# Kernel tuning notes

Hardware: AMD Instinct MI355X
Metric: run time of the kernel (lower is better)

Reference implementation:

```python
import math
import jax, jax.numpy as jnp
import numpy as np

D_MODEL = 256
N_HEADS = 4
HEAD_DIM = D_MODEL // N_HEADS
MAX_REL = 30


def _rel_pos_encodings(t, d_model):
    # sinusoidal table over clipped relative distances -> [t, t, d_model]
    n = 2 * MAX_REL + 1
    positions = jnp.arange(n, dtype=jnp.float32)[:, None]
    div_term = jnp.exp(jnp.arange(0, d_model, 2, dtype=jnp.float32) * (-math.log(10000.0) / d_model))
    ang = positions * div_term                      # [n, d/2]
    enc = jnp.stack([jnp.sin(ang), jnp.cos(ang)], axis=-1).reshape(n, d_model)
    rng = jnp.arange(t)
    final_mat = jnp.clip(rng[None, :] - rng[:, None], -MAX_REL, MAX_REL) + MAX_REL  # [t, t]
    return enc[final_mat]                           # [t, t, d_model]


def setup_inputs() -> dict:
    key = jax.random.key(0)
    ks = jax.random.split(key, 12)
    d = D_MODEL
    s = 1.0 / math.sqrt(d)
    inp = {
        "inputs": jax.random.normal(ks[0], (16, 512, d), dtype=jnp.float32),
        "ln_gamma": jnp.ones((d,), jnp.float32),
        "ln_beta": jnp.zeros((d,), jnp.float32),
        "Wq": jax.random.normal(ks[1], (d, d), jnp.float32) * s,
        "bq": jnp.zeros((d,), jnp.float32),
        "Wk": jax.random.normal(ks[2], (d, d), jnp.float32) * s,
        "bk": jnp.zeros((d,), jnp.float32),
        "Wv": jax.random.normal(ks[3], (d, d), jnp.float32) * s,
        "bv": jnp.zeros((d,), jnp.float32),
        "Wpos": jax.random.normal(ks[4], (d, d), jnp.float32) * s,
        "bpos": jnp.zeros((d,), jnp.float32),
        "Wo": jax.random.normal(ks[5], (d, d), jnp.float32) * s,
        "bo": jnp.zeros((d,), jnp.float32),
        "u_bias": jax.random.normal(ks[6], (1, N_HEADS, 1, HEAD_DIM), jnp.float32) * 0.02,
        "v_bias": jax.random.normal(ks[7], (1, N_HEADS, 1, HEAD_DIM), jnp.float32) * 0.02,
    }
    return inp


def reference(inputs, ln_gamma, ln_beta, Wq, bq, Wk, bk, Wv, bv, Wpos, bpos, Wo, bo, u_bias, v_bias):
    b, t, d = inputs.shape
    h, hd = N_HEADS, HEAD_DIM
    # LayerNorm (eps=1e-5, torch default)
    mu = jnp.mean(inputs, axis=-1, keepdims=True)
    var = jnp.mean(jnp.square(inputs - mu), axis=-1, keepdims=True)
    x = (inputs - mu) * jax.lax.rsqrt(var + 1e-5) * ln_gamma + ln_beta

    def split_heads(y):
        return y.reshape(b, t, h, hd).transpose(0, 2, 1, 3)  # b h t d

    q = split_heads(x @ Wq.T + bq)
    k = split_heads(x @ Wk.T + bk)
    v = split_heads(x @ Wv.T + bv)

    rel = jax.lax.stop_gradient(_rel_pos_encodings(t, d))    # [t, t, d]
    pos = (rel @ Wpos.T + bpos).reshape(t, t, h, hd)         # [t1, t2, h, hd]

    qk_score = jnp.einsum('bhtd,bhsd->bhts', q + u_bias, k)
    pos_score = jnp.einsum('bhtd,tshd->bhts', q + v_bias, pos)
    scores = (qk_score + pos_score) / math.sqrt(hd)
    attn = jax.nn.softmax(scores, axis=-1)
    ctx = jnp.einsum('bhts,bhsd->bhtd', attn, v)
    ctx = ctx.transpose(0, 2, 1, 3).reshape(b, t, d)
    return ctx @ Wo.T + bo
```

## Files before the change

### kernel.cpp

```cpp
#include <hip/hip_runtime.h>
#include <hip/hip_bf16.h>
#include <math.h>

#define B 16
#define T 512
#define D 256
#define H 4
#define HD 64
#define MAXREL 30
#define NREL 61
#define M_ROWS (B*T)
#define QBLK 64

typedef __attribute__((ext_vector_type(8))) short bf16x8;
typedef __attribute__((ext_vector_type(4))) float f32x4;
typedef unsigned short ush;

__device__ inline ush f2b(float f) {
    __hip_bfloat16 h = __float2bfloat16(f);
    union { __hip_bfloat16 h; ush u; } c; c.h = h; return c.u;
}
__device__ inline float b2f(ush u) {
    union { ush u; __hip_bfloat16 h; } c; c.u = u; return __bfloat162float(c.h);
}
__device__ inline int swz(int row, int byteoff) {
    return row * 128 + (byteoff ^ ((row & 7) << 4));
}
__device__ inline int swz256(int row, int byteoff) {
    return row * 256 + (byteoff ^ ((row & 7) << 4));
}
__device__ inline int swz512(int row, int byteoff) {
    return row * 512 + (byteoff ^ ((row & 7) << 4));
}

#define SCL 0.1803368801111204f

__global__ __launch_bounds__(256) void prep_kernel(const float* __restrict__ x,
                                                   const float* __restrict__ gamma,
                                                   const float* __restrict__ beta,
                                                   ush* __restrict__ xb,
                                                   const float* __restrict__ Wq, const float* __restrict__ Wk,
                                                   const float* __restrict__ Wv, const float* __restrict__ Wo,
                                                   ush* __restrict__ wb,
                                                   const float* __restrict__ Wpos,
                                                   const float* __restrict__ bpos,
                                                   ush* __restrict__ pospb) {
    __shared__ __attribute__((aligned(16))) ush wpS[64 * 256];
    int bid = blockIdx.x;
    int tid = threadIdx.x;
    if (bid < 2048) {
        int row = bid * 4 + (tid >> 6);
        int lane = tid & 63;
        const float* xr = x + (size_t)row * D;
        float4 v = *(const float4*)(xr + lane * 4);
        float s = v.x + v.y + v.z + v.w;
        #pragma unroll
        for (int off = 32; off; off >>= 1) s += __shfl_xor(s, off);
        float mu = s * (1.f / 256.f);
        float dx = v.x - mu, dy = v.y - mu, dz = v.z - mu, dw = v.w - mu;
        float vs = dx*dx + dy*dy + dz*dz + dw*dw;
        #pragma unroll
        for (int off = 32; off; off >>= 1) vs += __shfl_xor(vs, off);
        float rstd = rsqrtf(vs * (1.f / 256.f) + 1e-5f);
        float4 g = *(const float4*)(gamma + lane * 4);
        float4 bb = *(const float4*)(beta + lane * 4);
        ushort4 o;
        o.x = f2b(dx * rstd * g.x + bb.x);
        o.y = f2b(dy * rstd * g.y + bb.y);
        o.z = f2b(dz * rstd * g.z + bb.z);
        o.w = f2b(dw * rstd * g.w + bb.w);
        *(ushort4*)(xb + (size_t)row * D + lane * 4) = o;
    } else if (bid < 2048 + 256) {
        int b2 = bid - 2048;
        int z = b2 >> 6, xblk = b2 & 63;
        const float* src = z == 0 ? Wq : z == 1 ? Wk : z == 2 ? Wv : Wo;
        int idx = (xblk * 256 + tid) * 4;
        float4 v = *(const float4*)(src + idx);
        ushort4 o;
        o.x = f2b(v.x); o.y = f2b(v.y); o.z = f2b(v.z); o.w = f2b(v.w);
        *(ushort4*)(wb + (size_t)z * 65536 + idx) = o;
    } else {
        int h = bid - 2304;
        int w = tid >> 6, l = tid & 63, lg = l >> 4, ln = l & 15;
        const float* wsrc = Wpos + (size_t)(h * 64) * D;
        #pragma unroll
        for (int c = 0; c < 16; ++c) {
            int idx = c * 256 + tid;
            int row = idx >> 6, col = (idx & 63) * 4;
            float4 v = *(const float4*)(wsrc + (size_t)row * D + col);
            ushort4 o; o.x = f2b(v.x); o.y = f2b(v.y); o.z = f2b(v.z); o.w = f2b(v.w);
            *(ushort4*)((char*)wpS + swz512(row, col * 2)) = o;
        }
        int p = w * 16 + ln;
        bf16x8 af[8];
        #pragma unroll
        for (int ks = 0; ks < 8; ++ks) {
            #pragma unroll
            for (int j = 0; j < 8; ++j) {
                int k = ks * 32 + lg * 8 + j;
                int i = k >> 1;
                float dt = __expf(-(2.f * i) * (9.210340371976184f / 256.f));
                float ang = (float)p * dt;
                float v = (k & 1) ? __cosf(ang) : __sinf(ang);
                af[ks][j] = (short)f2b(v);
            }
        }
        __syncthreads();
        f32x4 acc[4] = {};
        #pragma unroll
        for (int ks = 0; ks < 8; ++ks) {
            int kbyte = (ks * 32 + lg * 8) * 2;
            #pragma unroll
            for (int ct = 0; ct < 4; ++ct) {
                bf16x8 bf = *(const bf16x8*)((const char*)wpS + swz512(ct * 16 + ln, kbyte));
                acc[ct] = __builtin_amdgcn_mfma_f32_16x16x32_bf16(af[ks], bf, acc[ct], 0, 0, 0);
            }
        }
        #pragma unroll
        for (int ct = 0; ct < 4; ++ct) {
            int dcol = ct * 16 + ln;
            float bb = bpos[h * 64 + dcol];
            #pragma unroll
            for (int r = 0; r < 4; ++r) {
                int pr = w * 16 + lg * 4 + r;
                pospb[(size_t)h * 4096 + pr * 64 + dcol] = f2b(acc[ct][r] + bb);
            }
        }
    }
}

#define PROJ_CORE \
    f32x4 acc[4][4] = {}; \
    { const ush* Ap = A + (size_t)i0 * D; \
      const ush* Wp = W + (size_t)j0 * D; \
      _Pragma("unroll 1") \
      for (int kb2 = 0; kb2 < 2; ++kb2) { \
        int k0 = kb2 * 128; \
        if (kb2) __syncthreads(); \
        _Pragma("unroll") \
        for (int c = 0; c < 8; ++c) { \
            int ci = c * 256 + tid; \
            int row = ci >> 4, sub = ci & 15; \
            *(bf16x8*)((char*)A_s + swz256(row, sub * 16)) = *(const bf16x8*)(Ap + (size_t)row * D + k0 + sub * 8); \
            *(bf16x8*)((char*)B_s + swz256(row, sub * 16)) = *(const bf16x8*)(Wp + (size_t)row * D + k0 + sub * 8); \
        } \
        __syncthreads(); \
        const char* aSrc = swap ? (const char*)A_s : (const char*)B_s; \
        const char* bSrc = swap ? (const char*)B_s : (const char*)A_s; \
        __builtin_amdgcn_s_setprio(1); \
        _Pragma("unroll") \
        for (int ksub = 0; ksub < 4; ++ksub) { \
            int kbyte = ksub * 64 + (l >> 4) * 16; \
            bf16x8 af[4], bfr[4]; \
            _Pragma("unroll") \
            for (int mi = 0; mi < 4; ++mi) af[mi]  = *(const bf16x8*)(aSrc + swz256(wr * 64 + mi * 16 + (l & 15), kbyte)); \
            _Pragma("unroll") \
            for (int ni = 0; ni < 4; ++ni) bfr[ni] = *(const bf16x8*)(bSrc + swz256(wc * 64 + ni * 16 + (l & 15), kbyte)); \
            _Pragma("unroll") \
            for (int mi = 0; mi < 4; ++mi) \
                _Pragma("unroll") \
                for (int ni = 0; ni < 4; ++ni) \
                    acc[mi][ni] = __builtin_amdgcn_mfma_f32_16x16x32_bf16(af[mi], bfr[ni], acc[mi][ni], 0, 0, 0); \
        } \
        __builtin_amdgcn_s_setprio(0); \
      } }

__global__ __launch_bounds__(256, 2) void qkv_mfma(const ush* __restrict__ A,
                                                   const ush* __restrict__ wball,
                                                   const float* __restrict__ bq,
                                                   const float* __restrict__ bk,
                                                   const float* __restrict__ bv,
                                                   ush* __restrict__ qb,
                                                   ush* __restrict__ kbuf,
                                                   ush* __restrict__ vtb) {
    __shared__ __attribute__((aligned(16))) ush A_s[128 * 128];
    __shared__ __attribute__((aligned(16))) ush B_s[128 * 128];
    int tid = threadIdx.x;
    int w = tid >> 6, l = tid & 63;
    int wr = w >> 1, wc = w & 1;
    int i0 = blockIdx.x * 128, j0 = blockIdx.y * 128;
    int z = blockIdx.z;
    const ush* W = wball + (size_t)z * 65536;
    const float* bias = z == 0 ? bq : (z == 1 ? bk : bv);
    int swap = (z == 2) ? 1 : 0;
    PROJ_CORE
    if (swap) {
        #pragma unroll
        for (int mi = 0; mi < 4; ++mi) {
            int t = i0 + wr * 64 + mi * 16 + (l >> 4) * 4;
            #pragma unroll
            for (int ni = 0; ni < 4; ++ni) {
                int j = j0 + wc * 64 + ni * 16 + (l & 15);
                float bvv = bias[j];
                ushort4 o;
                o.x = f2b(acc[mi][ni][0] + bvv); o.y = f2b(acc[mi][ni][1] + bvv);
                o.z = f2b(acc[mi][ni][2] + bvv); o.w = f2b(acc[mi][ni][3] + bvv);
                *(ushort4*)(vtb + (size_t)j * M_ROWS + t) = o;
            }
        }
    } else {
        ush* ob = (z == 0) ? qb : kbuf;
        #pragma unroll
        for (int mi = 0; mi < 4; ++mi) {
            int jb = j0 + wr * 64 + mi * 16 + (l >> 4) * 4;
            float4 bv4 = *(const float4*)(bias + jb);
            #pragma unroll
            for (int ni = 0; ni < 4; ++ni) {
                int t = i0 + wc * 64 + ni * 16 + (l & 15);
                ushort4 o;
                o.x = f2b(acc[mi][ni][0] + bv4.x); o.y = f2b(acc[mi][ni][1] + bv4.y);
                o.z = f2b(acc[mi][ni][2] + bv4.z); o.w = f2b(acc[mi][ni][3] + bv4.w);
                *(ushort4*)(ob + (size_t)t * D + jb) = o;
            }
        }
    }
}

__global__ __launch_bounds__(256, 2) void outproj_mfma(const ush* __restrict__ A,
                                                       const ush* __restrict__ W,
                                                       const float* __restrict__ bias,
                                                       float* __restrict__ of) {
    __shared__ __attribute__((aligned(16))) ush A_s[128 * 128];
    __shared__ __attribute__((aligned(16))) ush B_s[128 * 128];
    int tid = threadIdx.x;
    int w = tid >> 6, l = tid & 63;
    int wr = w >> 1, wc = w & 1;
    int i0 = blockIdx.x * 128, j0 = blockIdx.y * 128;
    const int swap = 0;
    PROJ_CORE
    #pragma unroll
    for (int mi = 0; mi < 4; ++mi) {
        int jb = j0 + wr * 64 + mi * 16 + (l >> 4) * 4;
        float4 bv4 = *(const float4*)(bias + jb);
        #pragma unroll
        for (int ni = 0; ni < 4; ++ni) {
            int t = i0 + wc * 64 + ni * 16 + (l & 15);
            float4 o;
            o.x = acc[mi][ni][0] + bv4.x; o.y = acc[mi][ni][1] + bv4.y;
            o.z = acc[mi][ni][2] + bv4.z; o.w = acc[mi][ni][3] + bv4.w;
            *(float4*)(of + (size_t)t * D + jb) = o;
        }
    }
}

__global__ __launch_bounds__(256, 3) void attn_mfma(const ush* __restrict__ qb,
                                                    const ush* __restrict__ kb,
                                                    const ush* __restrict__ vtb,
                                                    const ush* __restrict__ pospb,
                                                    const float* __restrict__ u_bias,
                                                    const float* __restrict__ v_bias,
                                                    ush* __restrict__ ctxb) {
    __shared__ __attribute__((aligned(16))) ush Kd[2][64 * 64];
    __shared__ __attribute__((aligned(16))) ush Vd[2][64 * 64];
    __shared__ __attribute__((aligned(16))) ush pdS[4][16 * 66];
    __shared__ __attribute__((aligned(16))) ush PlS[4][16 * 64];

    int tid = threadIdx.x;
    int w = tid >> 6;
    int l = tid & 63;
    int lg = l >> 4, ln = l & 15;
    int bh = blockIdx.x;
    int b = bh >> 2, h = bh & 3;
    int t0 = blockIdx.y * QBLK;
    const size_t baseBH = ((size_t)b * T) * D + h * HD;

    bf16x8 qu[2], qv[2];
    {
        const ush* qrow = qb + baseBH + (size_t)(t0 + w * 16 + ln) * D;
        int c0 = lg * 8;
        #pragma unroll
        for (int ks = 0; ks < 2; ++ks) {
            bf16x8 ld = *(const bf16x8*)(qrow + ks * 32 + c0);
            float4 ub0 = *(const float4*)(u_bias + h * HD + ks * 32 + c0);
            float4 ub1 = *(const float4*)(u_bias + h * HD + ks * 32 + c0 + 4);
            float4 vb0 = *(const float4*)(v_bias + h * HD + ks * 32 + c0);
            float4 vb1 = *(const float4*)(v_bias + h * HD + ks * 32 + c0 + 4);
            float ubv[8] = {ub0.x,ub0.y,ub0.z,ub0.w,ub1.x,ub1.y,ub1.z,ub1.w};
            float vbv[8] = {vb0.x,vb0.y,vb0.z,vb0.w,vb1.x,vb1.y,vb1.z,vb1.w};
            #pragma unroll
            for (int j = 0; j < 8; ++j) {
                float f = b2f((ush)ld[j]);
                qu[ks][j] = (short)f2b((f + ubv[j]) * SCL);
                qv[ks][j] = (short)f2b((f + vbv[j]) * SCL);
            }
        }
    }

    int r0 = tid >> 3,          c0 = tid & 7;
    int r1 = (tid + 256) >> 3,  c1 = (tid + 256) & 7;
    const ush* kbase = kb + baseBH;
    const ush* vbase = vtb + (size_t)(h * HD) * M_ROWS + (size_t)b * T;
    const ush* pbase = pospb + (size_t)h * 4096;

    {
        bf16x8 pp0 = *(const bf16x8*)(pbase + r0 * 64 + c0 * 8);
        bf16x8 pp1 = *(const bf16x8*)(pbase + r1 * 64 + c1 * 8);
        bf16x8 k0 = *(const bf16x8*)(kbase + (size_t)r0 * D + c0 * 8);
        bf16x8 k1 = *(const bf16x8*)(kbase + (size_t)r1 * D + c1 * 8);
        bf16x8 v0 = *(const bf16x8*)(vbase + (size_t)r0 * M_ROWS + c0 * 8);
        bf16x8 v1 = *(const bf16x8*)(vbase + (size_t)r1 * M_ROWS + c1 * 8);
        *(bf16x8*)((char*)Kd[1] + swz(r0, c0 * 16)) = pp0;
        *(bf16x8*)((char*)Kd[1] + swz(r1, c1 * 16)) = pp1;
        *(bf16x8*)((char*)Kd[0] + swz(r0, c0 * 16)) = k0;
        *(bf16x8*)((char*)Kd[0] + swz(r1, c1 * 16)) = k1;
        *(bf16x8*)((char*)Vd[0] + swz(r0, c0 * 16)) = v0;
        *(bf16x8*)((char*)Vd[0] + swz(r1, c1 * 16)) = v1;
    }
    bf16x8 sk0 = *(const bf16x8*)(kbase + (size_t)(64 + r0) * D + c0 * 8);
    bf16x8 sk1 = *(const bf16x8*)(kbase + (size_t)(64 + r1) * D + c1 * 8);
    bf16x8 sv0 = *(const bf16x8*)(vbase + (size_t)r0 * M_ROWS + 64 + c0 * 8);
    bf16x8 sv1 = *(const bf16x8*)(vbase + (size_t)r1 * M_ROWS + 64 + c1 * 8);
    __syncthreads();

    ush* pdW = pdS[w];
    {
        f32x4 pacc[4] = {};
        #pragma unroll
        for (int ks = 0; ks < 2; ++ks)
            #pragma unroll
            for (int ct = 0; ct < 4; ++ct) {
                bf16x8 bf = *(const bf16x8*)((const char*)Kd[1] + swz(ct * 16 + ln, (ks * 32 + lg * 8) * 2));
                pacc[ct] = __builtin_amdgcn_mfma_f32_16x16x32_bf16(qv[ks], bf, pacc[ct], 0, 0, 0);
            }
        #pragma unroll
        for (int ct = 0; ct < 4; ++ct)
            #pragma unroll
            for (int r = 0; r < 4; ++r)
                pdW[(lg * 4 + r) * 66 + ct * 16 + ln] = f2b(pacc[ct][r]);
    }
    float pdlo[4], pdhi[4];
    #pragma unroll
    for (int r = 0; r < 4; ++r) {
        pdlo[r] = b2f(pdW[(lg * 4 + r) * 66 + 0]);
        pdhi[r] = b2f(pdW[(lg * 4 + r) * 66 + 60]);
    }
    __syncthreads();

    f32x4 lacc = {};
    f32x4 o_acc[4] = {};
    ush* pw = PlS[w];
    bf16x8 ones;
    #pragma unroll
    for (int j = 0; j < 8; ++j) ones[j] = (short)0x3F80;
    int cur = 0;

    for (int st = 0; st < 8; ++st) {
        int s0 = st * 64;
        if (st < 7) {
            char* kdst = (char*)Kd[cur ^ 1];
            char* vdst = (char*)Vd[cur ^ 1];
            *(bf16x8*)(kdst + swz(r0, c0 * 16)) = sk0;
            *(bf16x8*)(kdst + swz(r1, c1 * 16)) = sk1;
            *(bf16x8*)(vdst + swz(r0, c0 * 16)) = sv0;
            *(bf16x8*)(vdst + swz(r1, c1 * 16)) = sv1;
        }
        if (st < 6) {
            int sn = s0 + 128;
            sk0 = *(const bf16x8*)(kbase + (size_t)(sn + r0) * D + c0 * 8);
            sk1 = *(const bf16x8*)(kbase + (size_t)(sn + r1) * D + c1 * 8);
            sv0 = *(const bf16x8*)(vbase + (size_t)r0 * M_ROWS + sn + c0 * 8);
            sv1 = *(const bf16x8*)(vbase + (size_t)r1 * M_ROWS + sn + c1 * 8);
        }

        const char* Kc = (const char*)Kd[cur];
        const char* Vc = (const char*)Vd[cur];

        int dlt = s0 - t0;
        f32x4 sacc[4];
        if (dlt >= 128) {
            #pragma unroll
            for (int ct = 0; ct < 4; ++ct)
                #pragma unroll
                for (int r = 0; r < 4; ++r) sacc[ct][r] = pdhi[r];
        } else if (dlt <= -128) {
            #pragma unroll
            for (int ct = 0; ct < 4; ++ct)
                #pragma unroll
                for (int r = 0; r < 4; ++r) sacc[ct][r] = pdlo[r];
        } else {
            #pragma unroll
            for (int ct = 0; ct < 4; ++ct)
                #pragma unroll
                for (int r = 0; r < 4; ++r) sacc[ct][r] = 0.f;
        }

        __builtin_amdgcn_s_setprio(1);
        #pragma unroll
        for (int ks = 0; ks < 2; ++ks)
            #pragma unroll
            for (int ct = 0; ct < 4; ++ct) {
                bf16x8 bf = *(const bf16x8*)(Kc + swz(ct * 16 + ln, (ks * 32 + lg * 8) * 2));
                sacc[ct] = __builtin_amdgcn_mfma_f32_16x16x32_bf16(qu[ks], bf, sacc[ct], 0, 0, 0);
            }
        __builtin_amdgcn_s_setprio(0);

        if (dlt > -128 && dlt < 128) {
            #pragma unroll
            for (int ct = 0; ct < 4; ++ct) {
                int s_g = s0 + ct * 16 + ln;
                #pragma unroll
                for (int r = 0; r < 4; ++r) {
                    int t_glob = t0 + w * 16 + lg * 4 + r;
                    int rel = s_g - t_glob;
                    rel = rel < -MAXREL ? -MAXREL : (rel > MAXREL ? MAXREL : rel);
                    sacc[ct][r] += b2f(pdW[(lg * 4 + r) * 66 + rel + MAXREL]);
                }
            }
        }

        #pragma unroll
        for (int ct = 0; ct < 4; ++ct)
            #pragma unroll
            for (int r = 0; r < 4; ++r)
                sacc[ct][r] = exp2f(sacc[ct][r]);

        #pragma unroll
        for (int ct = 0; ct < 4; ++ct)
            #pragma unroll
            for (int r = 0; r < 4; ++r)
                *(ush*)((char*)pw + swz(lg * 4 + r, (ct * 16 + ln) * 2)) = f2b(sacc[ct][r]);

        __builtin_amdgcn_s_setprio(1);
        #pragma unroll
        for (int ks = 0; ks < 2; ++ks) {
            bf16x8 pa = *(const bf16x8*)((const char*)pw + swz(ln, (ks * 32 + lg * 8) * 2));
            #pragma unroll
            for (int cd = 0; cd < 4; ++cd) {
                bf16x8 bv8 = *(const bf16x8*)(Vc + swz(cd * 16 + ln, (ks * 32 + lg * 8) * 2));
                o_acc[cd] = __builtin_amdgcn_mfma_f32_16x16x32_bf16(pa, bv8, o_acc[cd], 0, 0, 0);
            }
            lacc = __builtin_amdgcn_mfma_f32_16x16x32_bf16(pa, ones, lacc, 0, 0, 0);
        }
        __builtin_amdgcn_s_setprio(0);

        __syncthreads();
        cur ^= 1;
    }

    float inv[4];
    #pragma unroll
    for (int r = 0; r < 4; ++r) inv[r] = 1.f / lacc[r];
    #pragma unroll
    for (int cd = 0; cd < 4; ++cd)
        #pragma unroll
        for (int r = 0; r < 4; ++r) {
            int t_loc = w * 16 + lg * 4 + r;
            ctxb[baseBH + (size_t)(t0 + t_loc) * D + cd * 16 + ln] = f2b(o_acc[cd][r] * inv[r]);
        }
}

extern "C" void kernel_launch(void* const* d_in, const int* in_sizes, int n_in,
                              void* d_out, int out_size, void* d_ws, size_t ws_size,
                              hipStream_t stream) {
    const float* inputs  = (const float*)d_in[0];
    const float* ln_g    = (const float*)d_in[1];
    const float* ln_b    = (const float*)d_in[2];
    const float* Wq      = (const float*)d_in[3];
    const float* bq      = (const float*)d_in[4];
    const float* Wk      = (const float*)d_in[5];
    const float* bk      = (const float*)d_in[6];
    const float* Wv      = (const float*)d_in[7];
    const float* bv      = (const float*)d_in[8];
    const float* Wpos    = (const float*)d_in[9];
    const float* bpos    = (const float*)d_in[10];
    const float* Wo      = (const float*)d_in[11];
    const float* bo      = (const float*)d_in[12];
    const float* u_bias  = (const float*)d_in[13];
    const float* v_bias  = (const float*)d_in[14];
    float* out = (float*)d_out;

    char* w = (char*)d_ws;
    ush* xb    = (ush*)w;  w += (size_t)M_ROWS * D * 2;
    ush* qb    = (ush*)w;  w += (size_t)M_ROWS * D * 2;
    ush* kbuf  = (ush*)w;  w += (size_t)M_ROWS * D * 2;
    ush* vtb   = (ush*)w;  w += (size_t)M_ROWS * D * 2;
    ush* ctxb  = (ush*)w;  w += (size_t)M_ROWS * D * 2;
    ush* wb    = (ush*)w;  w += (size_t)4 * 65536 * 2;
    ush* pospb = (ush*)w;  w += (size_t)4 * 64 * 64 * 2;

    prep_kernel<<<2048 + 256 + 4, 256, 0, stream>>>(inputs, ln_g, ln_b, xb,
                                                    Wq, Wk, Wv, Wo, wb,
                                                    Wpos, bpos, pospb);

    qkv_mfma<<<dim3(M_ROWS / 128, 2, 3), 256, 0, stream>>>(xb, wb, bq, bk, bv, qb, kbuf, vtb);

    attn_mfma<<<dim3(B * H, T / QBLK), 256, 0, stream>>>(qb, kbuf, vtb, pospb, u_bias, v_bias, ctxb);

    outproj_mfma<<<dim3(M_ROWS / 128, 2), 256, 0, stream>>>(ctxb, wb + 3 * 65536, bo, out);
}
```

Before: 46.57 us.

## Shrink projection GEMM tiles and transpose attention score MFMA operands

The QKV projection tile drops from 128x128 to 128x64 and the output projection tile to 64x64. This launches more blocks to fill the GPU and lets QKV target 3 blocks per CU, at the cost of lower reuse per block. In attention, the QK MFMA operands are swapped so each lane owns one query row. That makes the rel-pos bias lookup use a single row, lets the constant bias init be one scalar, and allows P to be stored to LDS as packed bf16 pairs. The V-transpose store is now per-element scalar writes, which may coalesce less well.

Result: faster. 42.51 us (-8.7%).

```diff
diff --git a/kernel.cpp b/kernel.cpp
--- a/kernel.cpp
+++ b/kernel.cpp
@@ -22,6 +22,10 @@
 }
 __device__ inline float b2f(ush u) {
     union { ush u; __hip_bfloat16 h; } c; c.u = u; return __bfloat162float(c.h);
+}
+__device__ inline unsigned int pk2(float a, float b) {
+    __hip_bfloat162 h = __float22bfloat162_rn(make_float2(a, b));
+    union { __hip_bfloat162 h; unsigned int u; } c; c.h = h; return c.u;
 }
 __device__ inline int swz(int row, int byteoff) {
     return row * 128 + (byteoff ^ ((row & 7) << 4));
@@ -129,43 +133,7 @@
     }
 }
 
-#define PROJ_CORE \
-    f32x4 acc[4][4] = {}; \
-    { const ush* Ap = A + (size_t)i0 * D; \
-      const ush* Wp = W + (size_t)j0 * D; \
-      _Pragma("unroll 1") \
-      for (int kb2 = 0; kb2 < 2; ++kb2) { \
-        int k0 = kb2 * 128; \
-        if (kb2) __syncthreads(); \
-        _Pragma("unroll") \
-        for (int c = 0; c < 8; ++c) { \
-            int ci = c * 256 + tid; \
-            int row = ci >> 4, sub = ci & 15; \
-            *(bf16x8*)((char*)A_s + swz256(row, sub * 16)) = *(const bf16x8*)(Ap + (size_t)row * D + k0 + sub * 8); \
-            *(bf16x8*)((char*)B_s + swz256(row, sub * 16)) = *(const bf16x8*)(Wp + (size_t)row * D + k0 + sub * 8); \
-        } \
-        __syncthreads(); \
-        const char* aSrc = swap ? (const char*)A_s : (const char*)B_s; \
-        const char* bSrc = swap ? (const char*)B_s : (const char*)A_s; \
-        __builtin_amdgcn_s_setprio(1); \
-        _Pragma("unroll") \
-        for (int ksub = 0; ksub < 4; ++ksub) { \
-            int kbyte = ksub * 64 + (l >> 4) * 16; \
-            bf16x8 af[4], bfr[4]; \
-            _Pragma("unroll") \
-            for (int mi = 0; mi < 4; ++mi) af[mi]  = *(const bf16x8*)(aSrc + swz256(wr * 64 + mi * 16 + (l & 15), kbyte)); \
-            _Pragma("unroll") \
-            for (int ni = 0; ni < 4; ++ni) bfr[ni] = *(const bf16x8*)(bSrc + swz256(wc * 64 + ni * 16 + (l & 15), kbyte)); \
-            _Pragma("unroll") \
-            for (int mi = 0; mi < 4; ++mi) \
-                _Pragma("unroll") \
-                for (int ni = 0; ni < 4; ++ni) \
-                    acc[mi][ni] = __builtin_amdgcn_mfma_f32_16x16x32_bf16(af[mi], bfr[ni], acc[mi][ni], 0, 0, 0); \
-        } \
-        __builtin_amdgcn_s_setprio(0); \
-      } }
-
-__global__ __launch_bounds__(256, 2) void qkv_mfma(const ush* __restrict__ A,
+__global__ __launch_bounds__(256, 3) void qkv_mfma(const ush* __restrict__ A,
                                                    const ush* __restrict__ wball,
                                                    const float* __restrict__ bq,
                                                    const float* __restrict__ bk,
@@ -174,39 +142,79 @@
                                                    ush* __restrict__ kbuf,
                                                    ush* __restrict__ vtb) {
     __shared__ __attribute__((aligned(16))) ush A_s[128 * 128];
-    __shared__ __attribute__((aligned(16))) ush B_s[128 * 128];
+    __shared__ __attribute__((aligned(16))) ush B_s[64 * 128];
     int tid = threadIdx.x;
     int w = tid >> 6, l = tid & 63;
+    int lg = l >> 4, ln = l & 15;
     int wr = w >> 1, wc = w & 1;
-    int i0 = blockIdx.x * 128, j0 = blockIdx.y * 128;
+    int i0 = blockIdx.x * 128;
+    int j0 = blockIdx.y * 64;
     int z = blockIdx.z;
-    const ush* W = wball + (size_t)z * 65536;
+    const ush* Wp = wball + (size_t)z * 65536 + (size_t)j0 * D;
+    const ush* Ap = A + (size_t)i0 * D;
     const float* bias = z == 0 ? bq : (z == 1 ? bk : bv);
-    int swap = (z == 2) ? 1 : 0;
-    PROJ_CORE
-    if (swap) {
-        #pragma unroll
-        for (int mi = 0; mi < 4; ++mi) {
-            int t = i0 + wr * 64 + mi * 16 + (l >> 4) * 4;
+    f32x4 acc[2][4] = {};
+
+    #pragma unroll 1
+    for (int kb2 = 0; kb2 < 2; ++kb2) {
+        int k0 = kb2 * 128;
+        if (kb2) __syncthreads();
+        #pragma unroll
+        for (int c = 0; c < 8; ++c) {
+            int u = c * 256 + tid;
+            int row = u >> 4, sub = u & 15;
+            *(bf16x8*)((char*)A_s + swz256(row, sub * 16)) = *(const bf16x8*)(Ap + (size_t)row * D + k0 + sub * 8);
+        }
+        #pragma unroll
+        for (int c = 0; c < 4; ++c) {
+            int u = c * 256 + tid;
+            int row = u >> 4, sub = u & 15;
+            *(bf16x8*)((char*)B_s + swz256(row, sub * 16)) = *(const bf16x8*)(Wp + (size_t)row * D + k0 + sub * 8);
+        }
+        __syncthreads();
+        __builtin_amdgcn_s_setprio(1);
+        #pragma unroll
+        for (int ksub = 0; ksub < 4; ++ksub) {
+            int kbyte = ksub * 64 + lg * 16;
+            bf16x8 af[2], bfr[4];
+            #pragma unroll
+            for (int mi = 0; mi < 2; ++mi)
+                af[mi] = *(const bf16x8*)((const char*)B_s + swz256(wr * 32 + mi * 16 + ln, kbyte));
+            #pragma unroll
+            for (int ni = 0; ni < 4; ++ni)
+                bfr[ni] = *(const bf16x8*)((const char*)A_s + swz256(wc * 64 + ni * 16 + ln, kbyte));
+            #pragma unroll
+            for (int mi = 0; mi < 2; ++mi)
+                #pragma unroll
+                for (int ni = 0; ni < 4; ++ni)
+                    acc[mi][ni] = __builtin_amdgcn_mfma_f32_16x16x32_bf16(af[mi], bfr[ni], acc[mi][ni], 0, 0, 0);
+        }
+        __builtin_amdgcn_s_setprio(0);
+    }
+
+    if (z == 2) {
+        #pragma unroll
+        for (int mi = 0; mi < 2; ++mi) {
+            int jb = j0 + wr * 32 + mi * 16 + lg * 4;
+            float4 bv4 = *(const float4*)(bias + jb);
+            float bvv[4] = {bv4.x, bv4.y, bv4.z, bv4.w};
             #pragma unroll
             for (int ni = 0; ni < 4; ++ni) {
-                int j = j0 + wc * 64 + ni * 16 + (l & 15);
-                float bvv = bias[j];
-                ushort4 o;
-                o.x = f2b(acc[mi][ni][0] + bvv); o.y = f2b(acc[mi][ni][1] + bvv);
-                o.z = f2b(acc[mi][ni][2] + bvv); o.w = f2b(acc[mi][ni][3] + bvv);
-                *(ushort4*)(vtb + (size_t)j * M_ROWS + t) = o;
+                int t = i0 + wc * 64 + ni * 16 + ln;
+                #pragma unroll
+                for (int r = 0; r < 4; ++r)
+                    vtb[(size_t)(jb + r) * M_ROWS + t] = f2b(acc[mi][ni][r] + bvv[r]);
             }
         }
     } else {
         ush* ob = (z == 0) ? qb : kbuf;
         #pragma unroll
-        for (int mi = 0; mi < 4; ++mi) {
-            int jb = j0 + wr * 64 + mi * 16 + (l >> 4) * 4;
+        for (int mi = 0; mi < 2; ++mi) {
+            int jb = j0 + wr * 32 + mi * 16 + lg * 4;
             float4 bv4 = *(const float4*)(bias + jb);
             #pragma unroll
             for (int ni = 0; ni < 4; ++ni) {
-                int t = i0 + wc * 64 + ni * 16 + (l & 15);
+                int t = i0 + wc * 64 + ni * 16 + ln;
                 ushort4 o;
                 o.x = f2b(acc[mi][ni][0] + bv4.x); o.y = f2b(acc[mi][ni][1] + bv4.y);
                 o.z = f2b(acc[mi][ni][2] + bv4.z); o.w = f2b(acc[mi][ni][3] + bv4.w);
@@ -220,21 +228,57 @@
                                                        const ush* __restrict__ W,
                                                        const float* __restrict__ bias,
                                                        float* __restrict__ of) {
-    __shared__ __attribute__((aligned(16))) ush A_s[128 * 128];
-    __shared__ __attribute__((aligned(16))) ush B_s[128 * 128];
+    __shared__ __attribute__((aligned(16))) ush A_s[64 * 128];
+    __shared__ __attribute__((aligned(16))) ush B_s[64 * 128];
     int tid = threadIdx.x;
     int w = tid >> 6, l = tid & 63;
+    int lg = l >> 4, ln = l & 15;
     int wr = w >> 1, wc = w & 1;
-    int i0 = blockIdx.x * 128, j0 = blockIdx.y * 128;
-    const int swap = 0;
-    PROJ_CORE
+    int i0 = blockIdx.x * 64;
+    int j0 = blockIdx.y * 64;
+    const ush* Ap = A + (size_t)i0 * D;
+    const ush* Wp = W + (size_t)j0 * D;
+    f32x4 acc[2][2] = {};
+
+    #pragma unroll 1
+    for (int kb2 = 0; kb2 < 2; ++kb2) {
+        int k0 = kb2 * 128;
+        if (kb2) __syncthreads();
+        #pragma unroll
+        for (int c = 0; c < 4; ++c) {
+            int u = c * 256 + tid;
+            int row = u >> 4, sub = u & 15;
+            *(bf16x8*)((char*)A_s + swz256(row, sub * 16)) = *(const bf16x8*)(Ap + (size_t)row * D + k0 + sub * 8);
+            *(bf16x8*)((char*)B_s + swz256(row, sub * 16)) = *(const bf16x8*)(Wp + (size_t)row * D + k0 + sub * 8);
+        }
+        __syncthreads();
+        __builtin_amdgcn_s_setprio(1);
+        #pragma unroll
+        for (int ksub = 0; ksub < 4; ++ksub) {
+            int kbyte = ksub * 64 + lg * 16;
+            bf16x8 af[2], bfr[2];
+            #pragma unroll
+            for (int mi = 0; mi < 2; ++mi)
+                af[mi] = *(const bf16x8*)((const char*)B_s + swz256(wr * 32 + mi * 16 + ln, kbyte));
+            #pragma unroll
+            for (int ni = 0; ni < 2; ++ni)
+                bfr[ni] = *(const bf16x8*)((const char*)A_s + swz256(wc * 32 + ni * 16 + ln, kbyte));
+            #pragma unroll
+            for (int mi = 0; mi < 2; ++mi)
+                #pragma unroll
+                for (int ni = 0; ni < 2; ++ni)
+                    acc[mi][ni] = __builtin_amdgcn_mfma_f32_16x16x32_bf16(af[mi], bfr[ni], acc[mi][ni], 0, 0, 0);
+        }
+        __builtin_amdgcn_s_setprio(0);
+    }
+
     #pragma unroll
-    for (int mi = 0; mi < 4; ++mi) {
-        int jb = j0 + wr * 64 + mi * 16 + (l >> 4) * 4;
+    for (int mi = 0; mi < 2; ++mi) {
+        int jb = j0 + wr * 32 + mi * 16 + lg * 4;
         float4 bv4 = *(const float4*)(bias + jb);
         #pragma unroll
-        for (int ni = 0; ni < 4; ++ni) {
-            int t = i0 + wc * 64 + ni * 16 + (l & 15);
+        for (int ni = 0; ni < 2; ++ni) {
+            int t = i0 + wc * 32 + ni * 16 + ln;
             float4 o;
             o.x = acc[mi][ni][0] + bv4.x; o.y = acc[mi][ni][1] + bv4.y;
             o.z = acc[mi][ni][2] + bv4.z; o.w = acc[mi][ni][3] + bv4.w;
@@ -328,12 +372,8 @@
             for (int r = 0; r < 4; ++r)
                 pdW[(lg * 4 + r) * 66 + ct * 16 + ln] = f2b(pacc[ct][r]);
     }
-    float pdlo[4], pdhi[4];
-    #pragma unroll
-    for (int r = 0; r < 4; ++r) {
-        pdlo[r] = b2f(pdW[(lg * 4 + r) * 66 + 0]);
-        pdhi[r] = b2f(pdW[(lg * 4 + r) * 66 + 60]);
-    }
+    float pdlo = b2f(pdW[ln * 66 + 0]);
+    float pdhi = b2f(pdW[ln * 66 + 60]);
     __syncthreads();
 
     f32x4 lacc = {};
@@ -366,44 +406,33 @@
         const char* Vc = (const char*)Vd[cur];
 
         int dlt = s0 - t0;
+        float cinit = (dlt >= 128) ? pdhi : ((dlt <= -128) ? pdlo : 0.f);
         f32x4 sacc[4];
-        if (dlt >= 128) {
-            #pragma unroll
-            for (int ct = 0; ct < 4; ++ct)
-                #pragma unroll
-                for (int r = 0; r < 4; ++r) sacc[ct][r] = pdhi[r];
-        } else if (dlt <= -128) {
-            #pragma unroll
-            for (int ct = 0; ct < 4; ++ct)
-                #pragma unroll
-                for (int r = 0; r < 4; ++r) sacc[ct][r] = pdlo[r];
-        } else {
-            #pragma unroll
-            for (int ct = 0; ct < 4; ++ct)
-                #pragma unroll
-                for (int r = 0; r < 4; ++r) sacc[ct][r] = 0.f;
-        }
+        #pragma unroll
+        for (int ct = 0; ct < 4; ++ct)
+            #pragma unroll
+            for (int r = 0; r < 4; ++r) sacc[ct][r] = cinit;
 
         __builtin_amdgcn_s_setprio(1);
         #pragma unroll
         for (int ks = 0; ks < 2; ++ks)
             #pragma unroll
             for (int ct = 0; ct < 4; ++ct) {
-                bf16x8 bf = *(const bf16x8*)(Kc + swz(ct * 16 + ln, (ks * 32 + lg * 8) * 2));
-                sacc[ct] = __builtin_amdgcn_mfma_f32_16x16x32_bf16(qu[ks], bf, sacc[ct], 0, 0, 0);
+                bf16x8 kf = *(const bf16x8*)(Kc + swz(ct * 16 + ln, (ks * 32 + lg * 8) * 2));
+                sacc[ct] = __builtin_amdgcn_mfma_f32_16x16x32_bf16(kf, qu[ks], sacc[ct], 0, 0, 0);
             }
         __builtin_amdgcn_s_setprio(0);
 
         if (dlt > -128 && dlt < 128) {
+            int t_glob = t0 + w * 16 + ln;
             #pragma unroll
             for (int ct = 0; ct < 4; ++ct) {
-                int s_g = s0 + ct * 16 + ln;
                 #pragma unroll
                 for (int r = 0; r < 4; ++r) {
-                    int t_glob = t0 + w * 16 + lg * 4 + r;
+                    int s_g = s0 + ct * 16 + lg * 4 + r;
                     int rel = s_g - t_glob;
                     rel = rel < -MAXREL ? -MAXREL : (rel > MAXREL ? MAXREL : rel);
-                    sacc[ct][r] += b2f(pdW[(lg * 4 + r) * 66 + rel + MAXREL]);
+                    sacc[ct][r] += b2f(pdW[ln * 66 + rel + MAXREL]);
                 }
             }
         }
@@ -417,8 +446,9 @@
         #pragma unroll
         for (int ct = 0; ct < 4; ++ct)
             #pragma unroll
-            for (int r = 0; r < 4; ++r)
-                *(ush*)((char*)pw + swz(lg * 4 + r, (ct * 16 + ln) * 2)) = f2b(sacc[ct][r]);
+            for (int rr = 0; rr < 2; ++rr)
+                *(unsigned int*)((char*)pw + swz(ln, (ct * 16 + lg * 4 + rr * 2) * 2)) =
+                    pk2(sacc[ct][rr * 2], sacc[ct][rr * 2 + 1]);
 
         __builtin_amdgcn_s_setprio(1);
         #pragma unroll
@@ -482,9 +512,9 @@
                                                     Wq, Wk, Wv, Wo, wb,
                                                     Wpos, bpos, pospb);
 
-    qkv_mfma<<<dim3(M_ROWS / 128, 2, 3), 256, 0, stream>>>(xb, wb, bq, bk, bv, qb, kbuf, vtb);
+    qkv_mfma<<<dim3(M_ROWS / 128, 4, 3), 256, 0, stream>>>(xb, wb, bq, bk, bv, qb, kbuf, vtb);
 
     attn_mfma<<<dim3(B * H, T / QBLK), 256, 0, stream>>>(qb, kbuf, vtb, pospb, u_bias, v_bias, ctxb);
 
-    outproj_mfma<<<dim3(M_ROWS / 128, 2), 256, 0, stream>>>(ctxb, wb + 3 * 65536, bo, out);
-}
+    outproj_mfma<<<dim3(M_ROWS / 64, 4), 256, 0, stream>>>(ctxb, wb + 3 * 65536, bo, out);
+}
```
